# Kernel optimization log

Hardware: AMD Instinct MI355X
Metric: run time of the kernel (lower is better)

Reference implementation:

```python
import jax, jax.numpy as jnp
import numpy as np

B = 2            # boxes per cell
C = 20           # classes
NE = B * 5 + C   # 30 channels per cell
LAMBDA_COORD = 5.0
LAMBDA_NOOBJ = 0.5
EPS = 1e-12
BATCH, S, = 4096, 14
S2 = S * S


def setup_inputs() -> dict:
    key = jax.random.key(0)
    k1, k2, k3 = jax.random.split(key, 3)
    pred = jax.random.normal(k1, (BATCH, S2 * NE), dtype=jnp.float32)
    tgt = jax.random.uniform(k2, (BATCH, S, S, NE), dtype=jnp.float32)
    flag = (jax.random.uniform(k3, (BATCH, S, S)) < 0.3).astype(jnp.float32)
    tgt = tgt.at[..., 5].set(flag)
    return {"pred_tensor": pred, "target_tensor": tgt}


def _corners(b):
    # [..., 5] boxes [x,y,w,h,c] -> corners [x1,y1,x2,y2] with wh SQUARED (YOLOv1 sqrt param)
    xy = b[..., :2]
    wh2 = b[..., 2:4] ** 2
    return jnp.concatenate([xy - wh2, xy + wh2], axis=-1)


def reference(pred_tensor, target_tensor):
    batch = target_tensor.shape[0]
    t = target_tensor.reshape(batch, -1, NE)   # [b, s2, 30]
    p = pred_tensor.reshape(batch, -1, NE)

    coord = (t[..., 5] > 0).astype(p.dtype)    # [b, s2] cells with objects
    noobj = (t[..., 5] == 0).astype(p.dtype)   # [b, s2] cells without

    # class loss (sum MSE over coord cells)
    class_loss = jnp.sum(coord[..., None] * (p[..., B * 5:] - t[..., B * 5:]) ** 2)

    # no-object confidence loss: conf channels at i*5+4 for each box
    conf_idx = jnp.arange(B) * 5 + 4
    noobj_loss = jnp.sum(noobj[..., None] * (p[..., conf_idx] - t[..., conf_idx]) ** 2)

    # per-cell boxes [b, s2, B, 5]
    pb = p[..., :B * 5].reshape(batch, -1, B, 5)
    tb = t[..., :B * 5].reshape(batch, -1, B, 5)

    # pairwise IoU per cell: pred rows (N) vs target cols (M), [b, s2, B, B]
    c1 = _corners(pb)
    c2 = _corners(tb)
    tl = jnp.maximum(c1[..., :, None, :2], c2[..., None, :, :2])
    br = jnp.minimum(c1[..., :, None, 2:], c2[..., None, :, 2:])
    wh = jnp.clip(br - tl, 0.0)
    inter = wh[..., 0] * wh[..., 1]
    a1 = (c1[..., 2] - c1[..., 0]) * (c1[..., 3] - c1[..., 1])
    a2 = (c2[..., 2] - c2[..., 0]) * (c2[..., 3] - c2[..., 1])
    union = a1[..., :, None] + a2[..., None, :] - inter
    iou = inter / jnp.maximum(union, EPS)

    # torch: iou.max(0) -> best pred row per target col; scatter rows into response mask
    max_idx = jnp.argmax(iou, axis=-2)                       # [b, s2, B]
    resp = (jax.nn.one_hot(max_idx, B, dtype=p.dtype).sum(-2) > 0).astype(p.dtype)
    resp = jax.lax.stop_gradient(resp)                       # mask is non-differentiable

    w = coord[..., None] * resp                              # [b, s2, B]
    contain_loss = jnp.sum(w * (pb[..., 4] - tb[..., 4]) ** 2)
    loc_loss = jnp.sum(w[..., None] * (pb[..., :4] - tb[..., :4]) ** 2)

    total = LAMBDA_COORD * loc_loss + contain_loss + LAMBDA_NOOBJ * noobj_loss + class_loss
    return total
```

## Files before the change

kernel.cpp:

```cpp
#include <hip/hip_runtime.h>
#include <stdint.h>

#define NE 30
#define NB 2
#define NCELL (4096 * 196)
#define CPB 64
#define NBLK (NCELL / CPB)
#define PRED_F4 (CPB * NE / 4)
#define TOT_F4 (2 * PRED_F4)
#define NSTAGE (TOT_F4 / 64)
#define LAMBDA_COORD 5.0f
#define LAMBDA_NOOBJ 0.5f
#define EPSF 1e-12f

__global__ __launch_bounds__(64) void yolo_cell_kernel(
    const float* __restrict__ pred,
    const float* __restrict__ tgt,
    float* __restrict__ partial)
{
    __shared__ float sbuf[2 * CPB * NE];

    const int lane = threadIdx.x;
    const int blk  = blockIdx.x;

    const float4* gp = reinterpret_cast<const float4*>(pred) + (size_t)blk * PRED_F4;
    const float4* gt = reinterpret_cast<const float4*>(tgt)  + (size_t)blk * PRED_F4;

    #pragma unroll
    for (int k = 0; k < NSTAGE; ++k) {
        const int f = k * 64 + lane;
        const float4* src = (f < PRED_F4) ? (gp + f) : (gt + (f - PRED_F4));
        __builtin_amdgcn_global_load_lds(
            (const __attribute__((address_space(1))) void*)src,
            (__attribute__((address_space(3))) void*)&sbuf[k * 256],
            16, 0, 0);
    }
    __syncthreads();

    const float* p = sbuf + lane * NE;
    const float* t = sbuf + CPB * NE + lane * NE;

    const float coord = (t[5] > 0.0f)  ? 1.0f : 0.0f;
    const float noobj = (t[5] == 0.0f) ? 1.0f : 0.0f;

    float cls = 0.0f;
    #pragma unroll
    for (int k = NB * 5; k < NE; ++k) {
        float d = p[k] - t[k];
        cls += d * d;
    }
    cls *= coord;

    float dconf0 = p[4] - t[4];
    float dconf1 = p[9] - t[9];
    float conf_sq0 = dconf0 * dconf0;
    float conf_sq1 = dconf1 * dconf1;
    float no = noobj * (conf_sq0 + conf_sq1);

    float c1[NB][4], c2[NB][4], a1[NB], a2[NB];
    #pragma unroll
    for (int i = 0; i < NB; ++i) {
        float x = p[i*5 + 0], y = p[i*5 + 1];
        float w2 = p[i*5 + 2] * p[i*5 + 2];
        float h2 = p[i*5 + 3] * p[i*5 + 3];
        c1[i][0] = x - w2; c1[i][1] = y - h2;
        c1[i][2] = x + w2; c1[i][3] = y + h2;
        a1[i] = (2.0f * w2) * (2.0f * h2);

        float tx = t[i*5 + 0], ty = t[i*5 + 1];
        float tw2 = t[i*5 + 2] * t[i*5 + 2];
        float th2 = t[i*5 + 3] * t[i*5 + 3];
        c2[i][0] = tx - tw2; c2[i][1] = ty - th2;
        c2[i][2] = tx + tw2; c2[i][3] = ty + th2;
        a2[i] = (2.0f * tw2) * (2.0f * th2);
    }

    float iou[NB][NB];
    #pragma unroll
    for (int i = 0; i < NB; ++i) {
        #pragma unroll
        for (int j = 0; j < NB; ++j) {
            float tlx = fmaxf(c1[i][0], c2[j][0]);
            float tly = fmaxf(c1[i][1], c2[j][1]);
            float brx = fminf(c1[i][2], c2[j][2]);
            float bry = fminf(c1[i][3], c2[j][3]);
            float wx = fmaxf(brx - tlx, 0.0f);
            float wy = fmaxf(bry - tly, 0.0f);
            float inter = wx * wy;
            float uni = a1[i] + a2[j] - inter;
            iou[i][j] = inter / fmaxf(uni, EPSF);
        }
    }

    bool m0 = iou[1][0] > iou[0][0];
    bool m1 = iou[1][1] > iou[0][1];
    float w0 = coord * ((!m0 || !m1) ? 1.0f : 0.0f);
    float w1 = coord * (( m0 ||  m1) ? 1.0f : 0.0f);

    float contain = w0 * conf_sq0 + w1 * conf_sq1;

    float loc0 = 0.0f, loc1 = 0.0f;
    #pragma unroll
    for (int k = 0; k < 4; ++k) {
        float d0 = p[k] - t[k];
        float d1 = p[5 + k] - t[5 + k];
        loc0 += d0 * d0;
        loc1 += d1 * d1;
    }
    float loc = w0 * loc0 + w1 * loc1;

    float cell = LAMBDA_COORD * loc + contain + LAMBDA_NOOBJ * no + cls;

    #pragma unroll
    for (int off = 32; off > 0; off >>= 1)
        cell += __shfl_down(cell, off, 64);

    if (lane == 0) partial[blk] = cell;
}

__global__ __launch_bounds__(256) void yolo_reduce_kernel(
    const float* __restrict__ partial,
    float* __restrict__ out)
{
    const int tid = threadIdx.x;
    float s = 0.0f;
    for (int i = tid; i < NBLK; i += 256)
        s += partial[i];

    #pragma unroll
    for (int off = 32; off > 0; off >>= 1)
        s += __shfl_down(s, off, 64);

    __shared__ float wsum[4];
    const int lane = tid & 63;
    const int wid  = tid >> 6;
    if (lane == 0) wsum[wid] = s;
    __syncthreads();
    if (tid == 0)
        out[0] = wsum[0] + wsum[1] + wsum[2] + wsum[3];
}

extern "C" void kernel_launch(void* const* d_in, const int* in_sizes, int n_in,
                              void* d_out, int out_size, void* d_ws, size_t ws_size,
                              hipStream_t stream) {
    const float* pred = (const float*)d_in[0];
    const float* tgt  = (const float*)d_in[1];
    float* out = (float*)d_out;
    float* partial = (float*)d_ws;

    hipLaunchKernelGGL(yolo_cell_kernel, dim3(NBLK), dim3(64), 0, stream,
                       pred, tgt, partial);
    hipLaunchKernelGGL(yolo_reduce_kernel, dim3(1), dim3(256), 0, stream,
                       partial, out);
}
```

Measured before the change: 45.74 us.

## Process multiple cell groups per block with double-buffered LDS prefetch

Each 64-thread block now loops over 8 groups of 64 cells instead of one, shrinking the grid by 8x. LDS is double-buffered so the async global-to-LDS load of the next group is issued before computing the current one, synchronised with explicit s_waitcnt vmcnt. The intent is to overlap memory and compute and to amortise block launch and partial-sum overhead. In exchange, each block uses twice the LDS, which caps resident blocks per CU, and the smaller grid may leave an uneven tail across CUs.

```diff
diff --git a/kernel.cpp b/kernel.cpp
--- a/kernel.cpp
+++ b/kernel.cpp
@@ -5,41 +5,18 @@
 #define NB 2
 #define NCELL (4096 * 196)
 #define CPB 64
-#define NBLK (NCELL / CPB)
 #define PRED_F4 (CPB * NE / 4)
-#define TOT_F4 (2 * PRED_F4)
-#define NSTAGE (TOT_F4 / 64)
+#define NSTAGE (2 * PRED_F4 / 64)
+#define GPB 8
+#define GRID (NCELL / (CPB * GPB))
+#define GROUP_FLOATS (2 * CPB * NE)
 #define LAMBDA_COORD 5.0f
 #define LAMBDA_NOOBJ 0.5f
 #define EPSF 1e-12f
 
-__global__ __launch_bounds__(64) void yolo_cell_kernel(
-    const float* __restrict__ pred,
-    const float* __restrict__ tgt,
-    float* __restrict__ partial)
+__device__ __forceinline__ float cell_loss(const float* __restrict__ p,
+                                           const float* __restrict__ t)
 {
-    __shared__ float sbuf[2 * CPB * NE];
-
-    const int lane = threadIdx.x;
-    const int blk  = blockIdx.x;
-
-    const float4* gp = reinterpret_cast<const float4*>(pred) + (size_t)blk * PRED_F4;
-    const float4* gt = reinterpret_cast<const float4*>(tgt)  + (size_t)blk * PRED_F4;
-
-    #pragma unroll
-    for (int k = 0; k < NSTAGE; ++k) {
-        const int f = k * 64 + lane;
-        const float4* src = (f < PRED_F4) ? (gp + f) : (gt + (f - PRED_F4));
-        __builtin_amdgcn_global_load_lds(
-            (const __attribute__((address_space(1))) void*)src,
-            (__attribute__((address_space(3))) void*)&sbuf[k * 256],
-            16, 0, 0);
-    }
-    __syncthreads();
-
-    const float* p = sbuf + lane * NE;
-    const float* t = sbuf + CPB * NE + lane * NE;
-
     const float coord = (t[5] > 0.0f)  ? 1.0f : 0.0f;
     const float noobj = (t[5] == 0.0f) ? 1.0f : 0.0f;
 
@@ -109,13 +86,55 @@
     }
     float loc = w0 * loc0 + w1 * loc1;
 
-    float cell = LAMBDA_COORD * loc + contain + LAMBDA_NOOBJ * no + cls;
+    return LAMBDA_COORD * loc + contain + LAMBDA_NOOBJ * no + cls;
+}
+
+__global__ __launch_bounds__(64) void yolo_cell_kernel(
+    const float* __restrict__ pred,
+    const float* __restrict__ tgt,
+    float* __restrict__ partial)
+{
+    __shared__ float sbuf[2][GROUP_FLOATS];
+
+    const int lane = threadIdx.x;
+    const size_t base_f4 = (size_t)blockIdx.x * GPB * PRED_F4;
+    const float4* gp = reinterpret_cast<const float4*>(pred) + base_f4;
+    const float4* gt = reinterpret_cast<const float4*>(tgt)  + base_f4;
+
+    auto stage = [&](int b, int g) {
+        const size_t goff = (size_t)g * PRED_F4;
+        #pragma unroll
+        for (int k = 0; k < NSTAGE; ++k) {
+            const int f = k * 64 + lane;
+            const float4* src = (f < PRED_F4) ? (gp + goff + f)
+                                              : (gt + goff + (f - PRED_F4));
+            __builtin_amdgcn_global_load_lds(
+                (const __attribute__((address_space(1))) void*)src,
+                (__attribute__((address_space(3))) void*)&sbuf[b][k * 256],
+                16, 0, 0);
+        }
+    };
+
+    stage(0, 0);
+
+    float acc = 0.0f;
+    #pragma unroll
+    for (int g = 0; g < GPB; ++g) {
+        const int b = g & 1;
+        if (g + 1 < GPB) {
+            stage(b ^ 1, g + 1);
+            asm volatile("s_waitcnt vmcnt(15)" ::: "memory");
+        } else {
+            asm volatile("s_waitcnt vmcnt(0)" ::: "memory");
+        }
+        acc += cell_loss(&sbuf[b][lane * NE], &sbuf[b][CPB * NE + lane * NE]);
+    }
 
     #pragma unroll
     for (int off = 32; off > 0; off >>= 1)
-        cell += __shfl_down(cell, off, 64);
+        acc += __shfl_down(acc, off, 64);
 
-    if (lane == 0) partial[blk] = cell;
+    if (lane == 0) partial[blockIdx.x] = acc;
 }
 
 __global__ __launch_bounds__(256) void yolo_reduce_kernel(
@@ -124,7 +143,8 @@
 {
     const int tid = threadIdx.x;
     float s = 0.0f;
-    for (int i = tid; i < NBLK; i += 256)
+    #pragma unroll
+    for (int i = tid; i < GRID; i += 256)
         s += partial[i];
 
     #pragma unroll
@@ -148,7 +168,7 @@
     float* out = (float*)d_out;
     float* partial = (float*)d_ws;
 
-    hipLaunchKernelGGL(yolo_cell_kernel, dim3(NBLK), dim3(64), 0, stream,
+    hipLaunchKernelGGL(yolo_cell_kernel, dim3(GRID), dim3(64), 0, stream,
                        pred, tgt, partial);
     hipLaunchKernelGGL(yolo_reduce_kernel, dim3(1), dim3(256), 0, stream,
                        partial, out);
```

Result: faster. 36.86 us (-19.4%).
